# Performance work log

Measured on AMD Instinct MI355X. Metric: run time of the kernel, lower is better.

The kernel has to match this reference:

```python
import jax, jax.numpy as jnp
import numpy as np
from jax import lax

EPS = 1e-5

def silu(x):
    return x * jax.nn.sigmoid(x)

def setup_inputs() -> dict:
    key = jax.random.key(0)
    ks = jax.random.split(key, 8)
    B, T, H, W = 8, 32, 128, 128
    x = jax.random.normal(ks[0], (B, 1, T, H, W), jnp.float32)
    w_spatial = jax.random.normal(ks[1], (3, 1, 3, 3), jnp.float32) * 0.3
    b_spatial = jax.random.normal(ks[2], (3,), jnp.float32) * 0.1
    w_temporal = jax.random.normal(ks[3], (3, 1, 7, 1), jnp.float32) * 0.3
    b_temporal = jax.random.normal(ks[4], (3,), jnp.float32) * 0.1
    sn_weight = jnp.ones((1, 3, 1, 1, 1), jnp.float32)
    sn_bias = jnp.zeros((1, 3, 1, 1, 1), jnp.float32)
    mean_weight = jnp.ones((3,), jnp.float32)
    var_weight = jnp.ones((3,), jnp.float32)
    w_kv_s = jax.random.normal(ks[5], (2, T), jnp.float32) * (1.0 / np.sqrt(T))
    w_kv_t = jax.random.normal(ks[6], (2, H * W), jnp.float32) * (1.0 / np.sqrt(H * W))
    return dict(x=x, w_spatial=w_spatial, b_spatial=b_spatial,
                w_temporal=w_temporal, b_temporal=b_temporal,
                sn_weight=sn_weight, sn_bias=sn_bias,
                mean_weight=mean_weight, var_weight=var_weight,
                w_kv_s=w_kv_s, w_kv_t=w_kv_t)

def reference(x, w_spatial, b_spatial, w_temporal, b_temporal,
              sn_weight, sn_bias, mean_weight, var_weight, w_kv_s, w_kv_t):
    b, _, t, h, w = x.shape
    C = 3
    # --- spatial cone: timeIsHidden -> Conv2d(1,3,3,pad=1) -> SiLU ---
    xs = x.transpose(0, 2, 1, 3, 4).reshape(b * t, 1, h, w)  # (b t) c h w
    y = lax.conv_general_dilated(xs, w_spatial, (1, 1), ((1, 1), (1, 1)))
    y = silu(y + b_spatial[None, :, None, None])
    y = y.reshape(b, t, C, h, w).transpose(0, 2, 1, 3, 4)  # [b,3,t,h,w]
    # --- temporal cone: spaceIsHidden -> depthwise Conv2d(3,3,(7,1),groups=3) -> SiLU ---
    # kernel is (7,1) so convolving [b,3,t,hw] along t with width-1 in hw is identical math
    yt = y.reshape(b, C, t, h * w)
    z = lax.conv_general_dilated(yt, w_temporal, (1, 1), ((3, 3), (0, 0)),
                                 feature_group_count=C)
    z = silu(z + b_temporal[None, :, None, None]).reshape(b, C, t, h, w)
    # --- gain stage 1: SiLU + SwitchNorm3d(3) (training-mode statistics) ---
    g = silu(z)
    xr = g.reshape(b, C, -1)
    mean_in = xr.mean(-1, keepdims=True)              # [b,C,1] instance stats
    var_in = xr.var(-1, ddof=1, keepdims=True)        # torch .var is unbiased
    temp = var_in + mean_in ** 2
    mean_ln = mean_in.mean(1, keepdims=True)          # layer stats
    var_ln = temp.mean(1, keepdims=True) - mean_ln ** 2
    mean_bn = mean_in.mean(0, keepdims=True)          # batch stats
    var_bn = temp.mean(0, keepdims=True) - mean_bn ** 2
    mw = jax.nn.softmax(mean_weight)
    vw = jax.nn.softmax(var_weight)
    mean = mw[0] * mean_in + mw[1] * mean_ln + mw[2] * mean_bn
    var = vw[0] * var_in + vw[1] * var_ln + vw[2] * var_bn
    xn = ((xr - mean) / jnp.sqrt(var + EPS)).reshape(b, C, t, h, w)
    xn = xn * sn_weight + sn_bias
    # --- gain stage 2: GainControl (spatial/temporal kv via 1x1 convs) ---
    hw = h * w
    # to_kv_spatial: Conv2d(t,2,1,bias=False) over time-as-channel == contraction over t
    kv_s = jnp.einsum('bcthw,ot->bcohw', xn, w_kv_s)   # [b,C,2,h,w]
    ks_ = jax.nn.softmax(kv_s[:, :, 0].reshape(b, C, hw), axis=-1)[:, :, None, :]
    vs_ = kv_s[:, :, 1].reshape(b, C, hw)[:, :, None, :]
    # to_kv_temporal: Conv2d(hw,2,1,bias=False) over space-as-channel == contraction over hw
    xflat = xn.reshape(b, C, t, hw)
    kv_t = jnp.einsum('bcts,os->bcot', xflat, w_kv_t)  # [b,C,2,t]
    kt_ = jax.nn.softmax(kv_t[:, :, 0], axis=-1)[..., None]
    vt_ = kv_t[:, :, 1][..., None]
    out = jnp.sqrt(kt_ * ks_) * (vt_ * vs_)            # [b,C,t,hw]
    return out.reshape(b, C, t, h, w)
```

## Files before the change

kernel.cpp:

```cpp
#include <hip/hip_runtime.h>
#include <hip/hip_bf16.h>
#include <hip/hip_fp16.h>

#define Bn 8
#define Cn 3
#define Tn 32
#define Hn 128
#define Wn 128
#define HWn (Hn * Wn)
#define Nn (Tn * HWn)
#define EPSn 1e-5f
#define QT 2
#define SCH 128
#define SSW (SCH * QT)

__device__ __forceinline__ float silu_f(float v) {
    return v * __builtin_amdgcn_rcpf(1.0f + __expf(-v));
}

__global__ __launch_bounds__(256) void k1_spatial(
    const float* __restrict__ x, const float* __restrict__ wsp,
    const float* __restrict__ bsp, __half* __restrict__ y)
{
    const int tid = threadIdx.x;
    const int sub = tid & 31;
    const int bt = blockIdx.x;
    const int b = bt >> 5, t = bt & 31;
    const int row = blockIdx.y * 8 + (tid >> 5);
    const int col = sub * 4;

    float w[27], bb[3];
#pragma unroll
    for (int i = 0; i < 27; ++i) w[i] = wsp[i];
#pragma unroll
    for (int i = 0; i < 3; ++i) bb[i] = bsp[i];

    const float* xsl = x + ((size_t)b * Tn + t) * HWn + (size_t)row * Wn + col;
    const bool upok = row > 0, dnok = row < Hn - 1;
    const float4 z4 = make_float4(0.f, 0.f, 0.f, 0.f);
    float4 xm = upok ? *(const float4*)(xsl - Wn) : z4;
    float4 xc = *(const float4*)(xsl);
    float4 xp = dnok ? *(const float4*)(xsl + Wn) : z4;
    float xv[3][6];
    {
        float lu, rd;
        lu = __shfl_up(xm.w, 1);  rd = __shfl_down(xm.x, 1);
        xv[0][0] = (sub == 0) ? 0.f : lu; xv[0][1] = xm.x; xv[0][2] = xm.y;
        xv[0][3] = xm.z; xv[0][4] = xm.w; xv[0][5] = (sub == 31) ? 0.f : rd;
        lu = __shfl_up(xc.w, 1);  rd = __shfl_down(xc.x, 1);
        xv[1][0] = (sub == 0) ? 0.f : lu; xv[1][1] = xc.x; xv[1][2] = xc.y;
        xv[1][3] = xc.z; xv[1][4] = xc.w; xv[1][5] = (sub == 31) ? 0.f : rd;
        lu = __shfl_up(xp.w, 1);  rd = __shfl_down(xp.x, 1);
        xv[2][0] = (sub == 0) ? 0.f : lu; xv[2][1] = xp.x; xv[2][2] = xp.y;
        xv[2][3] = xp.z; xv[2][4] = xp.w; xv[2][5] = (sub == 31) ? 0.f : rd;
    }
#pragma unroll
    for (int c = 0; c < 3; ++c) {
        float s0 = bb[c], s1 = bb[c], s2 = bb[c], s3 = bb[c];
#pragma unroll
        for (int i = 0; i < 3; ++i) {
#pragma unroll
            for (int j = 0; j < 3; ++j) {
                const float wv = w[c * 9 + i * 3 + j];
                s0 += wv * xv[i][j];
                s1 += wv * xv[i][j + 1];
                s2 += wv * xv[i][j + 2];
                s3 += wv * xv[i][j + 3];
            }
        }
        __half2 o01 = __floats2half2_rn(silu_f(s0), silu_f(s1));
        __half2 o23 = __floats2half2_rn(silu_f(s2), silu_f(s3));
        __half2* dst = (__half2*)(y + ((size_t)(b * 3 + c) * Tn + t) * HWn
                                  + (size_t)row * Wn + col);
        dst[0] = o01; dst[1] = o23;
    }
}

template<int QTg>
__device__ __forceinline__ void k2_body(
    const __half* __restrict__ y, const float* __restrict__ wtp,
    const float* __restrict__ btp, const float* __restrict__ wkt,
    const float* __restrict__ wks,
    float* __restrict__ raw0, float* __restrict__ raw1,
    float* __restrict__ pt0p, float* __restrict__ pt1p,
    float* __restrict__ ss0p, float* __restrict__ ss1p)
{
    constexpr int O0 = QTg * 16;
    constexpr int O1 = O0 + 16;
    constexpr int SLO = (O0 - 3 < 0) ? 0 : (O0 - 3);
    constexpr int SHI = (O1 + 2 > Tn - 1) ? (Tn - 1) : (O1 + 2);

    const int tid = threadIdx.x, lane = tid & 63, wave = tid >> 6;
    const int sch = blockIdx.x * 2 + wave;
    const int bc  = blockIdx.y;
    const int c = bc % 3;
    const int s0i = sch * 128 + lane * 2;

    float wt_r[7];
#pragma unroll
    for (int i = 0; i < 7; ++i) wt_r[i] = wtp[c * 7 + i];
    const float bt_r = btp[c];

    const __half* yb = y + (size_t)bc * Nn + s0i;
    const float2 k0v = *(const float2*)(wkt + s0i);
    const float2 k1v = *(const float2*)(wkt + HWn + s0i);

    float2 ring[7];
    float2 a0 = make_float2(0.f, 0.f), a1 = make_float2(0.f, 0.f);
    float ps = 0.f, pq = 0.f;

#pragma unroll
    for (int tt = SLO; tt <= SHI + 3; ++tt) {
        if (tt <= SHI) {
            const __half2 hv = *(const __half2*)(yb + (size_t)tt * HWn);
            ring[tt % 7] = __half22float2(hv);
        }
        const int to = tt - 3;
        if (to >= O0 && to < O1) {
            float t0 = bt_r, t1 = bt_r;
#pragma unroll
            for (int k = 0; k < 7; ++k) {
                const int ts = to + k - 3;
                if (ts >= 0 && ts < Tn) {
                    const float wv = wt_r[k];
                    t0 += wv * ring[ts % 7].x;
                    t1 += wv * ring[ts % 7].y;
                }
            }
            const float g0 = silu_f(silu_f(t0));
            const float g1 = silu_f(silu_f(t1));
            const float wk0 = wks[to];
            const float wk1 = wks[Tn + to];
            a0.x += wk0 * g0; a0.y += wk0 * g1;
            a1.x += wk1 * g0; a1.y += wk1 * g1;
            ps += g0 + g1;
            pq += g0 * g0 + g1 * g1;
            float p0 = k0v.x * g0 + k0v.y * g1;
            float p1 = k1v.x * g0 + k1v.y * g1;
            p0 += __shfl_xor(p0, 1, 64); p0 += __shfl_xor(p0, 2, 64); p0 += __shfl_xor(p0, 4, 64);
            p1 += __shfl_xor(p1, 1, 64); p1 += __shfl_xor(p1, 2, 64); p1 += __shfl_xor(p1, 4, 64);
            float r = (lane & 1) ? p1 : p0;
            r += __shfl_xor(r, 8, 64);
            r += __shfl_xor(r, 16, 64);
            r += __shfl_xor(r, 32, 64);
            if (lane < 2) {
                float* dst = lane ? pt1p : pt0p;
                dst[((size_t)bc * Tn + to) * SCH + sch] = r;
            }
        }
    }

    {
        float p0 = ps, p1 = pq;
        p0 += __shfl_xor(p0, 1, 64); p0 += __shfl_xor(p0, 2, 64); p0 += __shfl_xor(p0, 4, 64);
        p1 += __shfl_xor(p1, 1, 64); p1 += __shfl_xor(p1, 2, 64); p1 += __shfl_xor(p1, 4, 64);
        float r = (lane & 1) ? p1 : p0;
        r += __shfl_xor(r, 8, 64);
        r += __shfl_xor(r, 16, 64);
        r += __shfl_xor(r, 32, 64);
        if (lane == 0) ss0p[(size_t)bc * SSW + sch * QT + QTg] = r;
        if (lane == 1) ss1p[(size_t)bc * SSW + sch * QT + QTg] = r;
    }
    {
        const size_t off = (size_t)(QTg * 24 + bc) * HWn + s0i;
        *(float2*)(raw0 + off) = a0;
        *(float2*)(raw1 + off) = a1;
    }
}

__global__ __launch_bounds__(128) void k2_temporal(
    const __half* __restrict__ y, const float* __restrict__ wtp,
    const float* __restrict__ btp, const float* __restrict__ wkt,
    const float* __restrict__ wks,
    float* __restrict__ raw0, float* __restrict__ raw1,
    float* __restrict__ pt0p, float* __restrict__ pt1p,
    float* __restrict__ ss0p, float* __restrict__ ss1p)
{
    if (blockIdx.z == 0)
        k2_body<0>(y, wtp, btp, wkt, wks, raw0, raw1, pt0p, pt1p, ss0p, ss1p);
    else
        k2_body<1>(y, wtp, btp, wkt, wks, raw0, raw1, pt0p, pt1p, ss0p, ss1p);
}

__global__ __launch_bounds__(256) void k3a_reduce(
    const float* __restrict__ pt0p, const float* __restrict__ pt1p,
    const float* __restrict__ ss0p, const float* __restrict__ ss1p,
    const float* __restrict__ wkt, const float* __restrict__ wks,
    float* __restrict__ kvt0r, float* __restrict__ kvt1r,
    float* __restrict__ ssS, float* __restrict__ ssSS, float* __restrict__ wsum)
{
    const int blk = blockIdx.x;
    const int tid = threadIdx.x;
    if (blk < Bn * Cn) {
        const int t = tid >> 3, g = tid & 7;
        const float4* p0 = (const float4*)(pt0p + ((size_t)blk * Tn + t) * SCH) + g * 4;
        const float4* p1 = (const float4*)(pt1p + ((size_t)blk * Tn + t) * SCH) + g * 4;
        float4 A0 = p0[0], A1 = p0[1], A2 = p0[2], A3 = p0[3];
        float4 B0 = p1[0], B1 = p1[1], B2 = p1[2], B3 = p1[3];
        float s0 = ((A0.x + A0.y) + (A0.z + A0.w)) + ((A1.x + A1.y) + (A1.z + A1.w))
                 + ((A2.x + A2.y) + (A2.z + A2.w)) + ((A3.x + A3.y) + (A3.z + A3.w));
        float s1 = ((B0.x + B0.y) + (B0.z + B0.w)) + ((B1.x + B1.y) + (B1.z + B1.w))
                 + ((B2.x + B2.y) + (B2.z + B2.w)) + ((B3.x + B3.y) + (B3.z + B3.w));
        s0 += __shfl_xor(s0, 1, 64); s0 += __shfl_xor(s0, 2, 64); s0 += __shfl_xor(s0, 4, 64);
        s1 += __shfl_xor(s1, 1, 64); s1 += __shfl_xor(s1, 2, 64); s1 += __shfl_xor(s1, 4, 64);
        if (g == 0) { kvt0r[blk * Tn + t] = s0; kvt1r[blk * Tn + t] = s1; }
        const float4* q0 = (const float4*)(ss0p + (size_t)blk * SSW);
        const float4* q1 = (const float4*)(ss1p + (size_t)blk * SSW);
        float a = 0.f, bb = 0.f;
        if (tid < SSW / 4) {
            float4 a4 = q0[tid], b4 = q1[tid];
            a = (a4.x + a4.y) + (a4.z + a4.w);
            bb = (b4.x + b4.y) + (b4.z + b4.w);
        }
        __shared__ float r0[256], r1[256];
        r0[tid] = a; r1[tid] = bb;
        __syncthreads();
        for (int off = 128; off > 0; off >>= 1) {
            if (tid < off) { r0[tid] += r0[tid + off]; r1[tid] += r1[tid + off]; }
            __syncthreads();
        }
        if (tid == 0) { ssS[blk] = r0[0]; ssSS[blk] = r1[0]; }
    } else {
        const float4* w0 = (const float4*)wkt;
        const float4* w1 = (const float4*)(wkt + HWn);
        float l0 = 0.f, l1 = 0.f;
        for (int i = tid; i < HWn / 4; i += 256) {
            float4 t0 = w0[i], t1 = w1[i];
            l0 += (t0.x + t0.y) + (t0.z + t0.w);
            l1 += (t1.x + t1.y) + (t1.z + t1.w);
        }
        __shared__ float r0[256], r1[256];
        r0[tid] = l0; r1[tid] = l1;
        __syncthreads();
        for (int off = 128; off > 0; off >>= 1) {
            if (tid < off) { r0[tid] += r0[tid + off]; r1[tid] += r1[tid + off]; }
            __syncthreads();
        }
        if (tid == 0) { wsum[0] = r0[0]; wsum[1] = r1[0]; }
        if (tid < 64) {
            float v = wks[tid];
            v += __shfl_xor(v, 1, 64); v += __shfl_xor(v, 2, 64);
            v += __shfl_xor(v, 4, 64); v += __shfl_xor(v, 8, 64);
            v += __shfl_xor(v, 16, 64);
            if (tid == 0) wsum[2] = v;
            if (tid == 32) wsum[3] = v;
        }
    }
}

__global__ __launch_bounds__(256) void k6_fused(
    const float* __restrict__ raw0, const float* __restrict__ raw1,
    const float* __restrict__ kvt0r, const float* __restrict__ kvt1r,
    const float* __restrict__ ssS, const float* __restrict__ ssSS,
    const float* __restrict__ wsum, const float* __restrict__ mean_w,
    const float* __restrict__ var_w, const float* __restrict__ snw,
    const float* __restrict__ snb, float* __restrict__ out)
{
    const int ch = blockIdx.x;
    const int bc = blockIdx.y;
    const int tid = threadIdx.x, lane = tid & 63, wave = tid >> 6;
    const int b = bc / 3, c = bc % 3;
    const float Nf = (float)Nn;

    float mln = 0.f, tln = 0.f;
#pragma unroll
    for (int cc = 0; cc < 3; ++cc) {
        float S = ssS[b * 3 + cc], SS = ssSS[b * 3 + cc];
        float m = S / Nf;
        float v = (SS - S * m) / (Nf - 1.0f);
        mln += m; tln += v + m * m;
    }
    mln *= (1.0f / 3.0f); tln *= (1.0f / 3.0f);
    const float vln = tln - mln * mln;
    float mbn = 0.f, tbn = 0.f;
#pragma unroll
    for (int bb2 = 0; bb2 < 8; ++bb2) {
        float S = ssS[bb2 * 3 + c], SS = ssSS[bb2 * 3 + c];
        float m = S / Nf;
        float v = (SS - S * m) / (Nf - 1.0f);
        mbn += m; tbn += v + m * m;
    }
    mbn *= 0.125f; tbn *= 0.125f;
    const float vbn = tbn - mbn * mbn;
    const float S_own = ssS[bc], SS_own = ssSS[bc];
    const float mean_in = S_own / Nf;
    const float var_in = (SS_own - S_own * mean_in) / (Nf - 1.0f);
    float mw0, mw1, mw2, vw0, vw1, vw2;
    {
        float m0 = mean_w[0], m1 = mean_w[1], m2 = mean_w[2];
        float mm = fmaxf(m0, fmaxf(m1, m2));
        float e0 = __expf(m0 - mm), e1 = __expf(m1 - mm), e2 = __expf(m2 - mm);
        float inv = 1.0f / (e0 + e1 + e2);
        mw0 = e0 * inv; mw1 = e1 * inv; mw2 = e2 * inv;
    }
    {
        float v0 = var_w[0], v1 = var_w[1], v2 = var_w[2];
        float vm = fmaxf(v0, fmaxf(v1, v2));
        float e0 = __expf(v0 - vm), e1 = __expf(v1 - vm), e2 = __expf(v2 - vm);
        float inv = 1.0f / (e0 + e1 + e2);
        vw0 = e0 * inv; vw1 = e1 * inv; vw2 = e2 * inv;
    }
    const float mean = mw0 * mean_in + mw1 * mln + mw2 * mbn;
    const float var  = vw0 * var_in + vw1 * vln + vw2 * vbn;
    const float sc = snw[c] / sqrtf(var + EPSn);
    const float sf = snb[c] - mean * sc;
    const float c0 = sf * wsum[2], c1 = sf * wsum[3];
    const float Wt0 = wsum[0], Wt1 = wsum[1];

    __shared__ float aSh[Tn];
    if (tid < Tn) {
        float k0 = sc * kvt0r[bc * Tn + tid] + sf * Wt0;
        float k1 = sc * kvt1r[bc * Tn + tid] + sf * Wt1;
        float m = k0;
#pragma unroll
        for (int d = 1; d < 32; d <<= 1) m = fmaxf(m, __shfl_xor(m, d, 64));
        float e = __expf(k0 - m);
        float s = e;
#pragma unroll
        for (int d = 1; d < 32; d <<= 1) s += __shfl_xor(s, d, 64);
        aSh[tid] = sqrtf(e / s) * k1;
    }

    const float* p0a = raw0 + (size_t)bc * HWn;
    const float* p0b = p0a + (size_t)24 * HWn;
    float mloc = -3.4e38f;
#pragma unroll
    for (int i = 0; i < 16; ++i) {
        const int idx = tid * 4 + i * 1024;
        float4 u = *(const float4*)(p0a + idx);
        float4 v = *(const float4*)(p0b + idx);
        mloc = fmaxf(mloc, fmaxf(fmaxf(sc * (u.x + v.x) + c0, sc * (u.y + v.y) + c0),
                                 fmaxf(sc * (u.z + v.z) + c0, sc * (u.w + v.w) + c0)));
    }
#pragma unroll
    for (int d = 1; d < 64; d <<= 1) mloc = fmaxf(mloc, __shfl_xor(mloc, d, 64));
    __shared__ float wred[4];
    if (lane == 0) wred[wave] = mloc;
    __syncthreads();
    const float M = fmaxf(fmaxf(wred[0], wred[1]), fmaxf(wred[2], wred[3]));
    __syncthreads();
    float sloc = 0.f;
#pragma unroll
    for (int i = 0; i < 16; ++i) {
        const int idx = tid * 4 + i * 1024;
        float4 u = *(const float4*)(p0a + idx);
        float4 v = *(const float4*)(p0b + idx);
        sloc += __expf(sc * (u.x + v.x) + c0 - M) + __expf(sc * (u.y + v.y) + c0 - M)
              + __expf(sc * (u.z + v.z) + c0 - M) + __expf(sc * (u.w + v.w) + c0 - M);
    }
#pragma unroll
    for (int d = 1; d < 64; d <<= 1) sloc += __shfl_xor(sloc, d, 64);
    if (lane == 0) wred[wave] = sloc;
    __syncthreads();
    const float Sexp = (wred[0] + wred[1]) + (wred[2] + wred[3]);
    const float invS = __builtin_amdgcn_rcpf(Sexp);

    const int s = ch * 1024 + tid * 4;
    const float* p1a = raw1 + (size_t)bc * HWn;
    const float* p1b = p1a + (size_t)24 * HWn;
    float4 u0 = *(const float4*)(p0a + s), v0 = *(const float4*)(p0b + s);
    float4 u1 = *(const float4*)(p1a + s), v1 = *(const float4*)(p1b + s);
    float4 Bv;
    Bv.x = sqrtf(__expf(sc * (u0.x + v0.x) + c0 - M) * invS) * (sc * (u1.x + v1.x) + c1);
    Bv.y = sqrtf(__expf(sc * (u0.y + v0.y) + c0 - M) * invS) * (sc * (u1.y + v1.y) + c1);
    Bv.z = sqrtf(__expf(sc * (u0.z + v0.z) + c0 - M) * invS) * (sc * (u1.z + v1.z) + c1);
    Bv.w = sqrtf(__expf(sc * (u0.w + v0.w) + c0 - M) * invS) * (sc * (u1.w + v1.w) + c1);
    float* op = out + (size_t)bc * Nn + s;
#pragma unroll
    for (int t = 0; t < Tn; ++t) {
        const float av = aSh[t];
        float4 o; o.x = av * Bv.x; o.y = av * Bv.y; o.z = av * Bv.z; o.w = av * Bv.w;
        *(float4*)(op + (size_t)t * HWn) = o;
    }
}

extern "C" void kernel_launch(void* const* d_in, const int* in_sizes, int n_in,
                              void* d_out, int out_size, void* d_ws, size_t ws_size,
                              hipStream_t stream) {
    const float* x          = (const float*)d_in[0];
    const float* w_spatial  = (const float*)d_in[1];
    const float* b_spatial  = (const float*)d_in[2];
    const float* w_temporal = (const float*)d_in[3];
    const float* b_temporal = (const float*)d_in[4];
    const float* sn_weight  = (const float*)d_in[5];
    const float* sn_bias    = (const float*)d_in[6];
    const float* mean_weight= (const float*)d_in[7];
    const float* var_weight = (const float*)d_in[8];
    const float* w_kv_s     = (const float*)d_in[9];
    const float* w_kv_t     = (const float*)d_in[10];
    float* out = (float*)d_out;
    float* ws  = (float*)d_ws;

    __half* yh   = (__half*)ws;
    float* raw0  = ws + 6291456;
    float* raw1  = raw0 + (size_t)QT * Bn * Cn * HWn;
    float* pt0p  = raw1 + (size_t)QT * Bn * Cn * HWn;
    float* pt1p  = pt0p + (size_t)Bn * Cn * Tn * SCH;
    float* ss0p  = pt1p + (size_t)Bn * Cn * Tn * SCH;
    float* ss1p  = ss0p + (size_t)Bn * Cn * SSW;
    float* kvt0r = ss1p + (size_t)Bn * Cn * SSW;
    float* kvt1r = kvt0r + Bn * Cn * Tn;
    float* ssS   = kvt1r + Bn * Cn * Tn;
    float* ssSS  = ssS + 24;
    float* wsum  = ssSS + 24;

    k1_spatial<<<dim3(Bn * Tn, Hn / 8), 256, 0, stream>>>(x, w_spatial, b_spatial, yh);
    k2_temporal<<<dim3(SCH / 2, Bn * Cn, QT), 128, 0, stream>>>(yh, w_temporal,
                                                                b_temporal, w_kv_t,
                                                                w_kv_s, raw0, raw1,
                                                                pt0p, pt1p, ss0p, ss1p);
    k3a_reduce<<<Bn * Cn + 1, 256, 0, stream>>>(pt0p, pt1p, ss0p, ss1p, w_kv_t, w_kv_s,
                                                kvt0r, kvt1r, ssS, ssSS, wsum);
    k6_fused<<<dim3(16, Bn * Cn), 256, 0, stream>>>(raw0, raw1, kvt0r, kvt1r,
                                                    ssS, ssSS, wsum, mean_weight,
                                                    var_weight, sn_weight, sn_bias, out);
}
```

Before: 63.61 us.

## Split temporal pass into four time quarters and pre-reduce partial spatial sums

The temporal conv kernel now splits time into four 8-step chunks instead of two 16-step ones, with 256-thread blocks, so the grid has more parallel work. The per-step cross-lane reductions of the temporal kv products are batched into one reduction after the loop. Because there are now four partial spatial accumulators, extra blocks in the reduce kernel sum them into single v0s/v1s buffers, and the final kernel reads one array instead of two. The cost is a larger halo overhead (more redundant y loads per chunk) and extra workspace traffic for the partial sums.

```diff
diff --git a/kernel.cpp b/kernel.cpp
--- a/kernel.cpp
+++ b/kernel.cpp
@@ -10,7 +10,7 @@
 #define HWn (Hn * Wn)
 #define Nn (Tn * HWn)
 #define EPSn 1e-5f
-#define QT 2
+#define QT 4
 #define SCH 128
 #define SSW (SCH * QT)
 
@@ -85,13 +85,13 @@
     float* __restrict__ pt0p, float* __restrict__ pt1p,
     float* __restrict__ ss0p, float* __restrict__ ss1p)
 {
-    constexpr int O0 = QTg * 16;
-    constexpr int O1 = O0 + 16;
+    constexpr int O0 = QTg * 8;
+    constexpr int O1 = O0 + 8;
     constexpr int SLO = (O0 - 3 < 0) ? 0 : (O0 - 3);
     constexpr int SHI = (O1 + 2 > Tn - 1) ? (Tn - 1) : (O1 + 2);
 
     const int tid = threadIdx.x, lane = tid & 63, wave = tid >> 6;
-    const int sch = blockIdx.x * 2 + wave;
+    const int sch = blockIdx.x * 4 + wave;
     const int bc  = blockIdx.y;
     const int c = bc % 3;
     const int s0i = sch * 128 + lane * 2;
@@ -108,6 +108,7 @@
     float2 ring[7];
     float2 a0 = make_float2(0.f, 0.f), a1 = make_float2(0.f, 0.f);
     float ps = 0.f, pq = 0.f;
+    float pt0a[8], pt1a[8];
 
 #pragma unroll
     for (int tt = SLO; tt <= SHI + 3; ++tt) {
@@ -135,21 +136,35 @@
             a1.x += wk1 * g0; a1.y += wk1 * g1;
             ps += g0 + g1;
             pq += g0 * g0 + g1 * g1;
-            float p0 = k0v.x * g0 + k0v.y * g1;
-            float p1 = k1v.x * g0 + k1v.y * g1;
-            p0 += __shfl_xor(p0, 1, 64); p0 += __shfl_xor(p0, 2, 64); p0 += __shfl_xor(p0, 4, 64);
-            p1 += __shfl_xor(p1, 1, 64); p1 += __shfl_xor(p1, 2, 64); p1 += __shfl_xor(p1, 4, 64);
-            float r = (lane & 1) ? p1 : p0;
-            r += __shfl_xor(r, 8, 64);
-            r += __shfl_xor(r, 16, 64);
-            r += __shfl_xor(r, 32, 64);
-            if (lane < 2) {
-                float* dst = lane ? pt1p : pt0p;
-                dst[((size_t)bc * Tn + to) * SCH + sch] = r;
-            }
-        }
-    }
-
+            pt0a[to - O0] = k0v.x * g0 + k0v.y * g1;
+            pt1a[to - O0] = k1v.x * g0 + k1v.y * g1;
+        }
+    }
+
+#pragma unroll
+    for (int i = 0; i < 8; ++i) {
+        pt0a[i] += __shfl_xor(pt0a[i], 1, 64);
+        pt0a[i] += __shfl_xor(pt0a[i], 2, 64);
+        pt0a[i] += __shfl_xor(pt0a[i], 4, 64);
+        pt1a[i] += __shfl_xor(pt1a[i], 1, 64);
+        pt1a[i] += __shfl_xor(pt1a[i], 2, 64);
+        pt1a[i] += __shfl_xor(pt1a[i], 4, 64);
+    }
+    {
+        const int j = lane & 7;
+        float r0 = (j == 0) ? pt0a[0] : (j == 1) ? pt0a[1] : (j == 2) ? pt0a[2]
+                 : (j == 3) ? pt0a[3] : (j == 4) ? pt0a[4] : (j == 5) ? pt0a[5]
+                 : (j == 6) ? pt0a[6] : pt0a[7];
+        float r1 = (j == 0) ? pt1a[0] : (j == 1) ? pt1a[1] : (j == 2) ? pt1a[2]
+                 : (j == 3) ? pt1a[3] : (j == 4) ? pt1a[4] : (j == 5) ? pt1a[5]
+                 : (j == 6) ? pt1a[6] : pt1a[7];
+        r0 += __shfl_xor(r0, 8, 64); r0 += __shfl_xor(r0, 16, 64); r0 += __shfl_xor(r0, 32, 64);
+        r1 += __shfl_xor(r1, 8, 64); r1 += __shfl_xor(r1, 16, 64); r1 += __shfl_xor(r1, 32, 64);
+        if (lane < 8)
+            pt0p[((size_t)bc * Tn + O0 + lane) * SCH + sch] = r0;
+        else if (lane < 16)
+            pt1p[((size_t)bc * Tn + O0 + (lane & 7)) * SCH + sch] = r1;
+    }
     {
         float p0 = ps, p1 = pq;
         p0 += __shfl_xor(p0, 1, 64); p0 += __shfl_xor(p0, 2, 64); p0 += __shfl_xor(p0, 4, 64);
@@ -168,7 +183,7 @@
     }
 }
 
-__global__ __launch_bounds__(128) void k2_temporal(
+__global__ __launch_bounds__(256) void k2_temporal(
     const __half* __restrict__ y, const float* __restrict__ wtp,
     const float* __restrict__ btp, const float* __restrict__ wkt,
     const float* __restrict__ wks,
@@ -176,18 +191,22 @@
     float* __restrict__ pt0p, float* __restrict__ pt1p,
     float* __restrict__ ss0p, float* __restrict__ ss1p)
 {
-    if (blockIdx.z == 0)
-        k2_body<0>(y, wtp, btp, wkt, wks, raw0, raw1, pt0p, pt1p, ss0p, ss1p);
-    else
-        k2_body<1>(y, wtp, btp, wkt, wks, raw0, raw1, pt0p, pt1p, ss0p, ss1p);
+    switch (blockIdx.z) {
+    case 0: k2_body<0>(y, wtp, btp, wkt, wks, raw0, raw1, pt0p, pt1p, ss0p, ss1p); break;
+    case 1: k2_body<1>(y, wtp, btp, wkt, wks, raw0, raw1, pt0p, pt1p, ss0p, ss1p); break;
+    case 2: k2_body<2>(y, wtp, btp, wkt, wks, raw0, raw1, pt0p, pt1p, ss0p, ss1p); break;
+    default: k2_body<3>(y, wtp, btp, wkt, wks, raw0, raw1, pt0p, pt1p, ss0p, ss1p); break;
+    }
 }
 
 __global__ __launch_bounds__(256) void k3a_reduce(
     const float* __restrict__ pt0p, const float* __restrict__ pt1p,
     const float* __restrict__ ss0p, const float* __restrict__ ss1p,
     const float* __restrict__ wkt, const float* __restrict__ wks,
+    const float* __restrict__ raw0, const float* __restrict__ raw1,
     float* __restrict__ kvt0r, float* __restrict__ kvt1r,
-    float* __restrict__ ssS, float* __restrict__ ssSS, float* __restrict__ wsum)
+    float* __restrict__ ssS, float* __restrict__ ssSS, float* __restrict__ wsum,
+    float* __restrict__ v0s, float* __restrict__ v1s)
 {
     const int blk = blockIdx.x;
     const int tid = threadIdx.x;
@@ -220,7 +239,7 @@
             __syncthreads();
         }
         if (tid == 0) { ssS[blk] = r0[0]; ssSS[blk] = r1[0]; }
-    } else {
+    } else if (blk == Bn * Cn) {
         const float4* w0 = (const float4*)wkt;
         const float4* w1 = (const float4*)(wkt + HWn);
         float l0 = 0.f, l1 = 0.f;
@@ -245,11 +264,29 @@
             if (tid == 0) wsum[2] = v;
             if (tid == 32) wsum[3] = v;
         }
+    } else {
+        const int rs = blk - (Bn * Cn + 1);
+        const int bc = rs >> 3, sl = rs & 7;
+        const size_t idx = (size_t)bc * HWn + sl * 2048 + tid * 8;
+        float4 a0 = make_float4(0.f, 0.f, 0.f, 0.f), a1 = a0, b0 = a0, b1 = a0;
+#pragma unroll
+        for (int q = 0; q < QT; ++q) {
+            const float* p0 = raw0 + (size_t)q * 24 * HWn + idx;
+            const float* p1 = raw1 + (size_t)q * 24 * HWn + idx;
+            float4 t0 = ((const float4*)p0)[0], t1 = ((const float4*)p0)[1];
+            float4 u0 = ((const float4*)p1)[0], u1 = ((const float4*)p1)[1];
+            a0.x += t0.x; a0.y += t0.y; a0.z += t0.z; a0.w += t0.w;
+            a1.x += t1.x; a1.y += t1.y; a1.z += t1.z; a1.w += t1.w;
+            b0.x += u0.x; b0.y += u0.y; b0.z += u0.z; b0.w += u0.w;
+            b1.x += u1.x; b1.y += u1.y; b1.z += u1.z; b1.w += u1.w;
+        }
+        ((float4*)(v0s + idx))[0] = a0; ((float4*)(v0s + idx))[1] = a1;
+        ((float4*)(v1s + idx))[0] = b0; ((float4*)(v1s + idx))[1] = b1;
     }
 }
 
 __global__ __launch_bounds__(256) void k6_fused(
-    const float* __restrict__ raw0, const float* __restrict__ raw1,
+    const float* __restrict__ v0s, const float* __restrict__ v1s,
     const float* __restrict__ kvt0r, const float* __restrict__ kvt1r,
     const float* __restrict__ ssS, const float* __restrict__ ssSS,
     const float* __restrict__ wsum, const float* __restrict__ mean_w,
@@ -321,16 +358,14 @@
         aSh[tid] = sqrtf(e / s) * k1;
     }
 
-    const float* p0a = raw0 + (size_t)bc * HWn;
-    const float* p0b = p0a + (size_t)24 * HWn;
+    const float* p0a = v0s + (size_t)bc * HWn;
     float mloc = -3.4e38f;
 #pragma unroll
     for (int i = 0; i < 16; ++i) {
         const int idx = tid * 4 + i * 1024;
         float4 u = *(const float4*)(p0a + idx);
-        float4 v = *(const float4*)(p0b + idx);
-        mloc = fmaxf(mloc, fmaxf(fmaxf(sc * (u.x + v.x) + c0, sc * (u.y + v.y) + c0),
-                                 fmaxf(sc * (u.z + v.z) + c0, sc * (u.w + v.w) + c0)));
+        mloc = fmaxf(mloc, fmaxf(fmaxf(sc * u.x + c0, sc * u.y + c0),
+                                 fmaxf(sc * u.z + c0, sc * u.w + c0)));
     }
 #pragma unroll
     for (int d = 1; d < 64; d <<= 1) mloc = fmaxf(mloc, __shfl_xor(mloc, d, 64));
@@ -344,9 +379,8 @@
     for (int i = 0; i < 16; ++i) {
         const int idx = tid * 4 + i * 1024;
         float4 u = *(const float4*)(p0a + idx);
-        float4 v = *(const float4*)(p0b + idx);
-        sloc += __expf(sc * (u.x + v.x) + c0 - M) + __expf(sc * (u.y + v.y) + c0 - M)
-              + __expf(sc * (u.z + v.z) + c0 - M) + __expf(sc * (u.w + v.w) + c0 - M);
+        sloc += __expf(sc * u.x + c0 - M) + __expf(sc * u.y + c0 - M)
+              + __expf(sc * u.z + c0 - M) + __expf(sc * u.w + c0 - M);
     }
 #pragma unroll
     for (int d = 1; d < 64; d <<= 1) sloc += __shfl_xor(sloc, d, 64);
@@ -356,15 +390,13 @@
     const float invS = __builtin_amdgcn_rcpf(Sexp);
 
     const int s = ch * 1024 + tid * 4;
-    const float* p1a = raw1 + (size_t)bc * HWn;
-    const float* p1b = p1a + (size_t)24 * HWn;
-    float4 u0 = *(const float4*)(p0a + s), v0 = *(const float4*)(p0b + s);
-    float4 u1 = *(const float4*)(p1a + s), v1 = *(const float4*)(p1b + s);
+    float4 u0 = *(const float4*)(p0a + s);
+    float4 u1 = *(const float4*)(v1s + (size_t)bc * HWn + s);
     float4 Bv;
-    Bv.x = sqrtf(__expf(sc * (u0.x + v0.x) + c0 - M) * invS) * (sc * (u1.x + v1.x) + c1);
-    Bv.y = sqrtf(__expf(sc * (u0.y + v0.y) + c0 - M) * invS) * (sc * (u1.y + v1.y) + c1);
-    Bv.z = sqrtf(__expf(sc * (u0.z + v0.z) + c0 - M) * invS) * (sc * (u1.z + v1.z) + c1);
-    Bv.w = sqrtf(__expf(sc * (u0.w + v0.w) + c0 - M) * invS) * (sc * (u1.w + v1.w) + c1);
+    Bv.x = sqrtf(__expf(sc * u0.x + c0 - M) * invS) * (sc * u1.x + c1);
+    Bv.y = sqrtf(__expf(sc * u0.y + c0 - M) * invS) * (sc * u1.y + c1);
+    Bv.z = sqrtf(__expf(sc * u0.z + c0 - M) * invS) * (sc * u1.z + c1);
+    Bv.w = sqrtf(__expf(sc * u0.w + c0 - M) * invS) * (sc * u1.w + c1);
     float* op = out + (size_t)bc * Nn + s;
 #pragma unroll
     for (int t = 0; t < Tn; ++t) {
@@ -398,20 +430,24 @@
     float* pt1p  = pt0p + (size_t)Bn * Cn * Tn * SCH;
     float* ss0p  = pt1p + (size_t)Bn * Cn * Tn * SCH;
     float* ss1p  = ss0p + (size_t)Bn * Cn * SSW;
-    float* kvt0r = ss1p + (size_t)Bn * Cn * SSW;
+    float* v0s   = ss1p + (size_t)Bn * Cn * SSW;
+    float* v1s   = v0s + (size_t)Bn * Cn * HWn;
+    float* kvt0r = v1s + (size_t)Bn * Cn * HWn;
     float* kvt1r = kvt0r + Bn * Cn * Tn;
     float* ssS   = kvt1r + Bn * Cn * Tn;
     float* ssSS  = ssS + 24;
     float* wsum  = ssSS + 24;
 
     k1_spatial<<<dim3(Bn * Tn, Hn / 8), 256, 0, stream>>>(x, w_spatial, b_spatial, yh);
-    k2_temporal<<<dim3(SCH / 2, Bn * Cn, QT), 128, 0, stream>>>(yh, w_temporal,
+    k2_temporal<<<dim3(SCH / 4, Bn * Cn, QT), 256, 0, stream>>>(yh, w_temporal,
                                                                 b_temporal, w_kv_t,
                                                                 w_kv_s, raw0, raw1,
                                                                 pt0p, pt1p, ss0p, ss1p);
-    k3a_reduce<<<Bn * Cn + 1, 256, 0, stream>>>(pt0p, pt1p, ss0p, ss1p, w_kv_t, w_kv_s,
-                                                kvt0r, kvt1r, ssS, ssSS, wsum);
-    k6_fused<<<dim3(16, Bn * Cn), 256, 0, stream>>>(raw0, raw1, kvt0r, kvt1r,
+    k3a_reduce<<<Bn * Cn + 1 + 192, 256, 0, stream>>>(pt0p, pt1p, ss0p, ss1p,
+                                                      w_kv_t, w_kv_s, raw0, raw1,
+                                                      kvt0r, kvt1r, ssS, ssSS, wsum,
+                                                      v0s, v1s);
+    k6_fused<<<dim3(16, Bn * Cn), 256, 0, stream>>>(v0s, v1s, kvt0r, kvt1r,
                                                     ssS, ssSS, wsum, mean_weight,
                                                     var_weight, sn_weight, sn_bias, out);
 }
```

Result: faster. 55.44 us (-12.8%).
